# Optimization experiments

Measured on AMD Instinct MI355X. Metric: run time of the kernel, lower is better.

## Reference

```python
import jax, jax.numpy as jnp
import numpy as np

N = 100000
E = 1600000
CARDS = [1000, 100, 50, 10000]
EDIMS = [10, 6, 5, 18]  # emb_dim_from_card = clip(round(1.8*card**0.25), 4, 24)
NUM_IN = 32
HID = 128
EPS = 1e-5


def setup_inputs() -> dict:
    key = jax.random.key(0)
    ks = jax.random.split(key, 24)
    x_num = jax.random.normal(ks[0], (N, NUM_IN), dtype=jnp.float32)
    cols = [jax.random.randint(jax.random.fold_in(ks[1], j), (N,), 0, c) for j, c in enumerate(CARDS)]
    x_cat = jnp.stack(cols, axis=1)
    edge_index = jax.random.randint(ks[2], (2, E), 0, N)
    embs = {f"emb{j}": 0.02 * jax.random.normal(ks[3 + j], (c, d), dtype=jnp.float32)
            for j, (c, d) in enumerate(zip(CARDS, EDIMS))}
    in_dim = NUM_IN + sum(EDIMS)  # 71
    def lin(k, fi, fo):
        s = 1.0 / np.sqrt(fi)
        return jax.random.uniform(k, (fi, fo), jnp.float32, -s, s)
    params = dict(
        w_in=lin(ks[7], in_dim, HID), b_in=jnp.zeros((HID,), jnp.float32),
        w1l=lin(ks[8], HID, HID), b1l=jnp.zeros((HID,), jnp.float32), w1r=lin(ks[9], HID, HID),
        w2l=lin(ks[10], HID, HID), b2l=jnp.zeros((HID,), jnp.float32), w2r=lin(ks[11], HID, HID),
        g1=jnp.ones((HID,), jnp.float32), be1=jnp.zeros((HID,), jnp.float32),
        g2=jnp.ones((HID,), jnp.float32), be2=jnp.zeros((HID,), jnp.float32),
        wh1=lin(ks[12], HID, 64), bh1=jnp.zeros((64,), jnp.float32),
        wh2=lin(ks[13], 64, 1), bh2=jnp.zeros((1,), jnp.float32),
    )
    return {"x_num": x_num, "x_cat": x_cat, "edge_index": edge_index, **embs, **params}


def _layer_norm(x, g, b):
    mu = jnp.mean(x, axis=-1, keepdims=True)
    var = jnp.var(x, axis=-1, keepdims=True)
    return (x - mu) * jax.lax.rsqrt(var + EPS) * g + b


def _sage_conv(x, src, dst, wl, bl, wr):
    # PyG SAGEConv(mean): lin_l(mean_{j in N(i)} x_j) + lin_r(x_i)
    agg = jax.ops.segment_sum(x[src], dst, num_segments=N)
    cnt = jax.ops.segment_sum(jnp.ones((src.shape[0],), x.dtype), dst, num_segments=N)
    mean = agg / jnp.maximum(cnt, 1.0)[:, None]
    return mean @ wl + bl + x @ wr


def reference(x_num, x_cat, edge_index,
              emb0, emb1, emb2, emb3,
              w_in, b_in, w1l, b1l, w1r, w2l, b2l, w2r,
              g1, be1, g2, be2, wh1, bh1, wh2, bh2):
    # eval mode: dropout is identity
    zc = jnp.concatenate([emb0[x_cat[:, 0]], emb1[x_cat[:, 1]],
                          emb2[x_cat[:, 2]], emb3[x_cat[:, 3]]], axis=1)
    x = jnp.concatenate([x_num, zc], axis=1)
    x = jax.nn.relu(x @ w_in + b_in)
    src, dst = edge_index[0], edge_index[1]
    x1 = jax.nn.relu(_layer_norm(_sage_conv(x, src, dst, w1l, b1l, w1r), g1, be1))
    x = x + 0.5 * x1
    x2 = jax.nn.relu(_layer_norm(_sage_conv(x, src, dst, w2l, b2l, w2r), g2, be2))
    x = x + 0.5 * x2
    h = jax.nn.relu(x @ wh1 + bh1)
    return (h @ wh2 + bh2)[:, 0]
```

## Files before the change

kernel.cpp:

```cpp
#include <hip/hip_runtime.h>

#define HID 128

typedef __attribute__((ext_vector_type(8))) short short8;
typedef __attribute__((ext_vector_type(4))) float f32x4;

__device__ __forceinline__ float bf2f(unsigned short u) {
    unsigned int x = ((unsigned int)u) << 16;
    return __builtin_bit_cast(float, x);
}
__device__ __forceinline__ unsigned short f2bf(float f) {
    unsigned int u = __builtin_bit_cast(unsigned int, f);
    u += 0x7fffu + ((u >> 16) & 1u);
    return (unsigned short)(u >> 16);
}

__device__ __forceinline__ void prep_one(const float* __restrict__ s1, int k1,
    const float* __restrict__ s2, int N, int i,
    unsigned short* __restrict__ whi, unsigned short* __restrict__ wlo)
{
    int k = i / N, nn = i - k * N;
    float v = (k < k1) ? s1[(size_t)k * N + nn]
                       : (s2 ? s2[(size_t)(k - k1) * N + nn] : 0.f);
    unsigned short h = f2bf(v);
    unsigned short l = f2bf(v - bf2f(h));
    size_t o = ((size_t)(k >> 5) * N + nn) * 32 + (k & 31);
    whi[o] = h; wlo[o] = l;
}

__global__ __launch_bounds__(256) void k_prep(
    const float* __restrict__ w_in, const float* __restrict__ w1l,
    const float* __restrict__ w1r, const float* __restrict__ w2l,
    const float* __restrict__ w2r, const float* __restrict__ wh1,
    unsigned short* __restrict__ w0h, unsigned short* __restrict__ w0l,
    unsigned short* __restrict__ w1h, unsigned short* __restrict__ w1lo,
    unsigned short* __restrict__ w2h, unsigned short* __restrict__ w2lo,
    unsigned short* __restrict__ whh, unsigned short* __restrict__ whl,
    unsigned short* __restrict__ z1, unsigned short* __restrict__ z2,
    int* __restrict__ gCur)
{
    int b = blockIdx.x, t = threadIdx.x;
    if (b < 48) {
        prep_one(w_in, 71, nullptr, 128, b * 256 + t, w0h, w0l);
    } else if (b < 176) {
        prep_one(w1l, 128, w1r, 128, (b - 48) * 256 + t, w1h, w1lo);
    } else if (b < 304) {
        prep_one(w2l, 128, w2r, 128, (b - 176) * 256 + t, w2h, w2lo);
    } else if (b < 336) {
        prep_one(wh1, 128, nullptr, 64, (b - 304) * 256 + t, whh, whl);
    } else {
        z1[t] = 0; z2[t] = 0;
        gCur[t] = 0; gCur[t + 256] = 0;
    }
}

__global__ __launch_bounds__(256) void k_stack0(
    const float* __restrict__ xnum, const int* __restrict__ xcat,
    const float* __restrict__ e0, const float* __restrict__ e1,
    const float* __restrict__ e2, const float* __restrict__ e3,
    unsigned short* __restrict__ A0, int n)
{
    int g = blockIdx.x * 256 + threadIdx.x;
    int r = g / 6, c = g - r * 6;
    if (r >= n) return;
    int4 cc = ((const int4*)xcat)[r];
    float v[16];
    int base = c * 16;
    #pragma unroll
    for (int j = 0; j < 16; ++j) {
        int col = base + j;
        float val;
        if      (col < 32) val = xnum[(size_t)r * 32 + col];
        else if (col < 42) val = e0[(size_t)cc.x * 10 + (col - 32)];
        else if (col < 48) val = e1[(size_t)cc.y * 6  + (col - 42)];
        else if (col < 53) val = e2[(size_t)cc.z * 5  + (col - 48)];
        else if (col < 71) val = e3[(size_t)cc.w * 18 + (col - 53)];
        else               val = 0.f;
        v[j] = val;
    }
    unsigned int ph[8];
    #pragma unroll
    for (int j = 0; j < 8; ++j)
        ph[j] = (unsigned int)f2bf(v[2*j]) | ((unsigned int)f2bf(v[2*j+1]) << 16);
    unsigned int* dh = (unsigned int*)(A0 + (size_t)r * 96 + base);
    uint4 a; a.x = ph[0]; a.y = ph[1]; a.z = ph[2]; a.w = ph[3];
    uint4 b; b.x = ph[4]; b.y = ph[5]; b.z = ph[6]; b.w = ph[7];
    ((uint4*)dh)[0] = a; ((uint4*)dh)[1] = b;
}

__global__ __launch_bounds__(256) void k_part(const int* __restrict__ esrc,
    const int* __restrict__ edst, int* __restrict__ gCur, int2* __restrict__ ebuf,
    int ecount, int chunk, int cap)
{
    __shared__ int hist[512];
    __shared__ int base[512];
    int t = threadIdx.x;
    hist[t] = 0; hist[t + 256] = 0;
    __syncthreads();
    int start = blockIdx.x * chunk;
    int end = start + chunk < ecount ? start + chunk : ecount;
    for (int i = start + t; i < end; i += 256)
        atomicAdd(&hist[edst[i] >> 8], 1);
    __syncthreads();
    for (int bk = t; bk < 512; bk += 256) {
        int h = hist[bk];
        base[bk] = h ? atomicAdd(&gCur[bk], h) : 0;
        hist[bk] = 0;
    }
    __syncthreads();
    for (int i = start + t; i < end; i += 256) {
        int d = edst[i];
        int b = d >> 8;
        int slot = atomicAdd(&hist[b], 1);
        int pos = base[b] + slot;
        if (pos < cap)
            ebuf[(size_t)b * cap + pos] = make_int2(esrc[i], d);
    }
}

__global__ __launch_bounds__(512) void k_scanb(const int* __restrict__ gCur,
    int* __restrict__ bBase, int* __restrict__ row_ptr, int nbuck, int n, int ecount)
{
    __shared__ int sm[512];
    int t = threadIdx.x;
    int c = (t < nbuck) ? gCur[t] : 0;
    sm[t] = c;
    __syncthreads();
    for (int d = 1; d < 512; d <<= 1) {
        int v = (t >= d) ? sm[t - d] : 0;
        __syncthreads();
        sm[t] += v;
        __syncthreads();
    }
    if (t < nbuck) bBase[t] = sm[t] - c;
    if (t == 0) row_ptr[n] = ecount;
}

__global__ __launch_bounds__(256) void k_bcsr(const int2* __restrict__ ebuf,
    const int* __restrict__ gCur, const int* __restrict__ bBase,
    int* __restrict__ row_ptr, int* __restrict__ col, int cap, int n)
{
    __shared__ int h[256];
    __shared__ int sm[256];
    int b = blockIdx.x, t = threadIdx.x;
    int cnt = gCur[b];
    int nb0 = b << 8;
    const int2* eb = ebuf + (size_t)b * cap;
    h[t] = 0;
    __syncthreads();
    for (int i = t; i < cnt; i += 256)
        atomicAdd(&h[eb[i].y & 255], 1);
    __syncthreads();
    int hv = h[t];
    sm[t] = hv;
    __syncthreads();
    for (int d = 1; d < 256; d <<= 1) {
        int v = (t >= d) ? sm[t - d] : 0;
        __syncthreads();
        sm[t] += v;
        __syncthreads();
    }
    int excl = sm[t] - hv;
    int gb = bBase[b];
    int g = nb0 + t;
    if (g < n) row_ptr[g] = gb + excl;
    __syncthreads();
    h[t] = excl;
    __syncthreads();
    for (int i = t; i < cnt; i += 256) {
        int2 e = eb[i];
        int slot = atomicAdd(&h[e.y & 255], 1);
        col[gb + slot] = e.x;
    }
}

__global__ __launch_bounds__(256) void k_agg(
    const unsigned short* __restrict__ xh, unsigned short* __restrict__ mh, int SK,
    const int* __restrict__ row_ptr, const int* __restrict__ col, int n,
    int zr, int emax)
{
    int lane = threadIdx.x & 63;
    int qw  = lane >> 4;
    int l16 = lane & 15;
    int node = blockIdx.x * 4 + (threadIdx.x >> 6);
    if (node >= n) return;
    node = __builtin_amdgcn_readfirstlane(node);
    int s = row_ptr[node], e = row_ptr[node + 1];
    int deg = e - s;
    float a0 = 0.f, a1 = 0.f, a2 = 0.f, a3 = 0.f;
    float a4 = 0.f, a5 = 0.f, a6 = 0.f, a7 = 0.f;
    size_t cOff = (size_t)l16 * 8;

    auto accum = [&](uint4 r) {
        a0 += __builtin_bit_cast(float, r.x << 16);
        a1 += __builtin_bit_cast(float, r.x & 0xffff0000u);
        a2 += __builtin_bit_cast(float, r.y << 16);
        a3 += __builtin_bit_cast(float, r.y & 0xffff0000u);
        a4 += __builtin_bit_cast(float, r.z << 16);
        a5 += __builtin_bit_cast(float, r.z & 0xffff0000u);
        a6 += __builtin_bit_cast(float, r.w << 16);
        a7 += __builtin_bit_cast(float, r.w & 0xffff0000u);
    };

    int em1 = emax - 1;
    for (int p = s + qw; p < e; p += 16) {
        int p1 = p + 4, p2 = p + 8, p3 = p + 12;
        int q1 = p1 < em1 ? p1 : em1;
        int q2 = p2 < em1 ? p2 : em1;
        int q3 = p3 < em1 ? p3 : em1;
        int t0 = col[p];
        int t1 = col[q1];
        int t2 = col[q2];
        int t3 = col[q3];
        int c0 = t0;
        int c1 = (p1 < e) ? t1 : zr;
        int c2 = (p2 < e) ? t2 : zr;
        int c3 = (p3 < e) ? t3 : zr;
        uint4 r0 = *(const uint4*)(xh + (size_t)c0 * SK + cOff);
        uint4 r1 = *(const uint4*)(xh + (size_t)c1 * SK + cOff);
        uint4 r2 = *(const uint4*)(xh + (size_t)c2 * SK + cOff);
        uint4 r3 = *(const uint4*)(xh + (size_t)c3 * SK + cOff);
        accum(r0); accum(r1); accum(r2); accum(r3);
    }

    a0 += __shfl_xor(a0, 16); a0 += __shfl_xor(a0, 32);
    a1 += __shfl_xor(a1, 16); a1 += __shfl_xor(a1, 32);
    a2 += __shfl_xor(a2, 16); a2 += __shfl_xor(a2, 32);
    a3 += __shfl_xor(a3, 16); a3 += __shfl_xor(a3, 32);
    a4 += __shfl_xor(a4, 16); a4 += __shfl_xor(a4, 32);
    a5 += __shfl_xor(a5, 16); a5 += __shfl_xor(a5, 32);
    a6 += __shfl_xor(a6, 16); a6 += __shfl_xor(a6, 32);
    a7 += __shfl_xor(a7, 16); a7 += __shfl_xor(a7, 32);

    if (qw == 0) {
        float inv = 1.f / (float)(deg > 1 ? deg : 1);
        uint4 o;
        o.x = (unsigned int)f2bf(a0 * inv) | ((unsigned int)f2bf(a1 * inv) << 16);
        o.y = (unsigned int)f2bf(a2 * inv) | ((unsigned int)f2bf(a3 * inv) << 16);
        o.z = (unsigned int)f2bf(a4 * inv) | ((unsigned int)f2bf(a5 * inv) << 16);
        o.w = (unsigned int)f2bf(a6 * inv) | ((unsigned int)f2bf(a7 * inv) << 16);
        *(uint4*)(mh + (size_t)node * SK + cOff) = o;
    }
}

template<int NC, int KT8, int EPI>
__global__ __launch_bounds__(256) void k_gemm(
    const unsigned short* __restrict__ A, int SK,
    const unsigned short* __restrict__ Whi, const unsigned short* __restrict__ Wlo,
    const float* __restrict__ bias,
    const float* __restrict__ g, const float* __restrict__ be,
    const unsigned short* __restrict__ Src, int SSK,
    unsigned short* __restrict__ Dst, int DSK,
    const float* __restrict__ wh2, const float* __restrict__ bh2, float* __restrict__ outp,
    int n)
{
    constexpr int NT = NC / 64;
    __shared__ float Cb[32][NC + 4];
    int t = threadIdx.x;
    int lane = t & 63, w = t >> 6;
    int l15 = lane & 15, kg = lane >> 4;
    int m0 = blockIdx.x * 64;

    size_t aoff[4];
    #pragma unroll
    for (int mt = 0; mt < 4; ++mt) {
        int r = m0 + mt * 16 + l15;
        r = r < n ? r : n - 1;
        aoff[mt] = (size_t)r * SK + kg * 8;
    }
    size_t nb[NT];
    #pragma unroll
    for (int nt = 0; nt < NT; ++nt)
        nb[nt] = (size_t)(w * (NC / 4) + nt * 16 + l15) * 32 + kg * 8;

    f32x4 acc[4][NT];
    #pragma unroll
    for (int mt = 0; mt < 4; ++mt)
        #pragma unroll
        for (int nt = 0; nt < NT; ++nt)
            acc[mt][nt] = (f32x4)(0.f);

    #pragma unroll 1
    for (int s = 0; s < KT8; ++s) {
        int koff = s * 32;
        short8 ah[4];
        #pragma unroll
        for (int mt = 0; mt < 4; ++mt)
            ah[mt] = *(const short8*)(A + aoff[mt] + koff);
        short8 bh[NT], bl[NT];
        #pragma unroll
        for (int nt = 0; nt < NT; ++nt) {
            bh[nt] = *(const short8*)(Whi + (size_t)s * NC * 32 + nb[nt]);
            bl[nt] = *(const short8*)(Wlo + (size_t)s * NC * 32 + nb[nt]);
        }
        #pragma unroll
        for (int mt = 0; mt < 4; ++mt)
            #pragma unroll
            for (int nt = 0; nt < NT; ++nt)
                acc[mt][nt] = __builtin_amdgcn_mfma_f32_16x16x32_bf16(ah[mt], bh[nt], acc[mt][nt], 0, 0, 0);
        #pragma unroll
        for (int mt = 0; mt < 4; ++mt)
            #pragma unroll
            for (int nt = 0; nt < NT; ++nt)
                acc[mt][nt] = __builtin_amdgcn_mfma_f32_16x16x32_bf16(ah[mt], bl[nt], acc[mt][nt], 0, 0, 0);
    }

    constexpr int CW = NC / 8;
    int er = t >> 3, q = t & 7;
    int cb = q * CW;

    #pragma unroll
    for (int p = 0; p < 2; ++p) {
        if (p) __syncthreads();
        #pragma unroll
        for (int mt2 = 0; mt2 < 2; ++mt2) {
            int mt = 2 * p + mt2;
            #pragma unroll
            for (int nt = 0; nt < NT; ++nt)
                #pragma unroll
                for (int r = 0; r < 4; ++r)
                    Cb[mt2 * 16 + kg * 4 + r][w * (NC / 4) + nt * 16 + l15] = acc[mt][nt][r];
        }
        __syncthreads();

        int gr = m0 + p * 32 + er;

        if (EPI == 0) {
            if (gr < n) {
                #pragma unroll
                for (int i = 0; i < CW / 4; ++i) {
                    int c = cb + 4 * i;
                    float4 v  = *(const float4*)&Cb[er][c];
                    float4 bi = *(const float4*)&bias[c];
                    ushort4 hv = make_ushort4(f2bf(fmaxf(v.x + bi.x, 0.f)),
                                              f2bf(fmaxf(v.y + bi.y, 0.f)),
                                              f2bf(fmaxf(v.z + bi.z, 0.f)),
                                              f2bf(fmaxf(v.w + bi.w, 0.f)));
                    *(ushort4*)(Dst + (size_t)gr * DSK + c) = hv;
                }
            }
        } else if (EPI == 1) {
            float s = 0.f, ss = 0.f;
            #pragma unroll
            for (int i = 0; i < CW / 4; ++i) {
                int c = cb + 4 * i;
                float4 v  = *(const float4*)&Cb[er][c];
                float4 bi = *(const float4*)&bias[c];
                float a0 = v.x + bi.x, a1 = v.y + bi.y, a2 = v.z + bi.z, a3 = v.w + bi.w;
                s  += a0 + a1 + a2 + a3;
                ss += a0 * a0 + a1 * a1 + a2 * a2 + a3 * a3;
            }
            s  += __shfl_xor(s, 1);  s  += __shfl_xor(s, 2);  s  += __shfl_xor(s, 4);
            ss += __shfl_xor(ss, 1); ss += __shfl_xor(ss, 2); ss += __shfl_xor(ss, 4);
            float mu  = s * (1.f / NC);
            float var = ss * (1.f / NC) - mu * mu;
            float rs  = rsqrtf(var + 1e-5f);
            if (gr < n) {
                #pragma unroll
                for (int i = 0; i < CW / 4; ++i) {
                    int c = cb + 4 * i;
                    float4 v  = *(const float4*)&Cb[er][c];
                    float4 bi = *(const float4*)&bias[c];
                    float4 gg = *(const float4*)&g[c];
                    float4 bb = *(const float4*)&be[c];
                    float r0 = fmaxf((v.x + bi.x - mu) * rs * gg.x + bb.x, 0.f);
                    float r1 = fmaxf((v.y + bi.y - mu) * rs * gg.y + bb.y, 0.f);
                    float r2 = fmaxf((v.z + bi.z - mu) * rs * gg.z + bb.z, 0.f);
                    float r3 = fmaxf((v.w + bi.w - mu) * rs * gg.w + bb.w, 0.f);
                    ushort4 rh = *(const ushort4*)(Src + (size_t)gr * SSK + c);
                    ushort4 hv = make_ushort4(f2bf(bf2f(rh.x) + 0.5f * r0),
                                              f2bf(bf2f(rh.y) + 0.5f * r1),
                                              f2bf(bf2f(rh.z) + 0.5f * r2),
                                              f2bf(bf2f(rh.w) + 0.5f * r3));
                    *(ushort4*)(Dst + (size_t)gr * DSK + c) = hv;
                }
            }
        } else {
            float s = 0.f;
            #pragma unroll
            for (int i = 0; i < CW / 4; ++i) {
                int c = cb + 4 * i;
                float4 v  = *(const float4*)&Cb[er][c];
                float4 bi = *(const float4*)&bias[c];
                float4 w2 = *(const float4*)&wh2[c];
                s += fmaxf(v.x + bi.x, 0.f) * w2.x + fmaxf(v.y + bi.y, 0.f) * w2.y
                   + fmaxf(v.z + bi.z, 0.f) * w2.z + fmaxf(v.w + bi.w, 0.f) * w2.w;
            }
            s += __shfl_xor(s, 1); s += __shfl_xor(s, 2); s += __shfl_xor(s, 4);
            if (q == 0 && gr < n) outp[gr] = s + bh2[0];
        }
    }
}

extern "C" void kernel_launch(void* const* d_in, const int* in_sizes, int n_in,
                              void* d_out, int out_size, void* d_ws, size_t ws_size,
                              hipStream_t stream)
{
    const float* xnum = (const float*)d_in[0];
    const int*   xcat = (const int*)d_in[1];
    const int*   eidx = (const int*)d_in[2];
    const float* e0   = (const float*)d_in[3];
    const float* e1   = (const float*)d_in[4];
    const float* e2   = (const float*)d_in[5];
    const float* e3   = (const float*)d_in[6];
    const float* w_in = (const float*)d_in[7];
    const float* b_in = (const float*)d_in[8];
    const float* w1l  = (const float*)d_in[9];
    const float* b1l  = (const float*)d_in[10];
    const float* w1r  = (const float*)d_in[11];
    const float* w2l  = (const float*)d_in[12];
    const float* b2l  = (const float*)d_in[13];
    const float* w2r  = (const float*)d_in[14];
    const float* g1   = (const float*)d_in[15];
    const float* be1  = (const float*)d_in[16];
    const float* g2   = (const float*)d_in[17];
    const float* be2  = (const float*)d_in[18];
    const float* wh1  = (const float*)d_in[19];
    const float* bh1  = (const float*)d_in[20];
    const float* wh2  = (const float*)d_in[21];
    const float* bh2  = (const float*)d_in[22];

    int n = in_sizes[0] / 32;
    int ecount = in_sizes[2] / 2;
    const int* esrc = eidx;
    const int* edst = eidx + ecount;

    char* ws = (char*)d_ws;
    size_t off = 0;
    auto alloc = [&](size_t bytes) -> void* {
        void* p = ws + off;
        off += (bytes + 255) & ~(size_t)255;
        return p;
    };
    unsigned short* A1 = (unsigned short*)alloc((size_t)(n + 1) * 256 * 2);
    unsigned short* A3 = A1;
    unsigned short* A2 = (unsigned short*)alloc((size_t)(n + 1) * 256 * 2);
    unsigned short* A0 = A2;
    unsigned short* w0h = (unsigned short*)alloc((size_t)96 * 128 * 2);
    unsigned short* w0l = (unsigned short*)alloc((size_t)96 * 128 * 2);
    unsigned short* w1h = (unsigned short*)alloc((size_t)256 * 128 * 2);
    unsigned short* w1lo= (unsigned short*)alloc((size_t)256 * 128 * 2);
    unsigned short* w2h = (unsigned short*)alloc((size_t)256 * 128 * 2);
    unsigned short* w2lo= (unsigned short*)alloc((size_t)256 * 128 * 2);
    unsigned short* whh = (unsigned short*)alloc((size_t)128 * 64 * 2);
    unsigned short* whl = (unsigned short*)alloc((size_t)128 * 64 * 2);
    int nbuck = (n + 255) >> 8;
    int cap = ecount / nbuck + ecount / (2 * nbuck) + 256;
    int* gCur    = (int*)alloc(512 * 4);
    int* bBase   = (int*)alloc(512 * 4);
    int* row_ptr = (int*)alloc((size_t)(n + 1) * 4);
    int* col     = (int*)alloc((size_t)ecount * 4);
    int2* ebuf   = (int2*)alloc((size_t)nbuck * cap * 8);
    (void)ws_size; (void)n_in; (void)out_size;

    int gemmBlocks = (n + 63) / 64;
    int aggBlocks = (n + 3) / 4;

    k_prep<<<337, 256, 0, stream>>>(
        w_in, w1l, w1r, w2l, w2r, wh1,
        w0h, w0l, w1h, w1lo, w2h, w2lo, whh, whl,
        A1 + (size_t)n * 256, A2 + (size_t)n * 256, gCur);

    k_stack0<<<((size_t)n * 6 + 255) / 256, 256, 0, stream>>>(xnum, xcat, e0, e1, e2, e3, A0, n);

    int nblkP = 512;
    int chunk = (ecount + nblkP - 1) / nblkP;
    k_part<<<nblkP, 256, 0, stream>>>(esrc, edst, gCur, ebuf, ecount, chunk, cap);
    k_scanb<<<1, 512, 0, stream>>>(gCur, bBase, row_ptr, nbuck, n, ecount);
    k_bcsr<<<nbuck, 256, 0, stream>>>(ebuf, gCur, bBase, row_ptr, col, cap, n);

    k_gemm<128, 3, 0><<<gemmBlocks, 256, 0, stream>>>(
        A0, 96, w0h, w0l, b_in,
        nullptr, nullptr, nullptr, 0,
        A1 + 128, 256,
        nullptr, nullptr, nullptr, n);

    k_agg<<<aggBlocks, 256, 0, stream>>>(A1 + 128, A1, 256, row_ptr, col, n, n, ecount);
    k_gemm<128, 8, 1><<<gemmBlocks, 256, 0, stream>>>(
        A1, 256, w1h, w1lo, b1l,
        g1, be1, A1 + 128, 256,
        A2 + 128, 256,
        nullptr, nullptr, nullptr, n);

    k_agg<<<aggBlocks, 256, 0, stream>>>(A2 + 128, A2, 256, row_ptr, col, n, n, ecount);
    k_gemm<128, 8, 1><<<gemmBlocks, 256, 0, stream>>>(
        A2, 256, w2h, w2lo, b2l,
        g2, be2, A2 + 128, 256,
        A3, 128,
        nullptr, nullptr, nullptr, n);

    k_gemm<64, 4, 2><<<gemmBlocks, 256, 0, stream>>>(
        A3, 128, whh, whl, bh1,
        nullptr, nullptr, nullptr, 0,
        nullptr, 0,
        wh2, bh2, (float*)d_out, n);
}
```

Baseline: 434.3 us.

## Fuse head MLP into second SAGE layer GEMM epilogue

The final head GEMM kernel is folded into the epilogue of the layer-2 GEMM. The residual output tile stays in shared memory and is multiplied by the head weights with MFMA in-block, then reduced to the scalar output. This removes one kernel launch and the round trip of writing and re-reading the 100000x128 bf16 intermediate. The cost is extra shared memory, extra syncs per sub-tile, and more register pressure in the layer-2 kernel.

```diff
diff --git a/kernel.cpp b/kernel.cpp
--- a/kernel.cpp
+++ b/kernel.cpp
@@ -251,11 +251,15 @@
     const float* __restrict__ g, const float* __restrict__ be,
     const unsigned short* __restrict__ Src, int SSK,
     unsigned short* __restrict__ Dst, int DSK,
+    const unsigned short* __restrict__ Hh, const unsigned short* __restrict__ Hl,
+    const float* __restrict__ bh1p,
     const float* __restrict__ wh2, const float* __restrict__ bh2, float* __restrict__ outp,
     int n)
 {
     constexpr int NT = NC / 64;
     __shared__ float Cb[32][NC + 4];
+    __shared__ unsigned short Xs[(EPI == 3) ? 32 : 1][(EPI == 3) ? 132 : 1];
+    __shared__ float hq[(EPI == 3) ? 4 : 1][(EPI == 3) ? 32 : 1];
     int t = threadIdx.x;
     int lane = t & 63, w = t >> 6;
     int l15 = lane & 15, kg = lane >> 4;
@@ -339,7 +343,7 @@
                     *(ushort4*)(Dst + (size_t)gr * DSK + c) = hv;
                 }
             }
-        } else if (EPI == 1) {
+        } else {
             float s = 0.f, ss = 0.f;
             #pragma unroll
             for (int i = 0; i < CW / 4; ++i) {
@@ -355,7 +359,8 @@
             float mu  = s * (1.f / NC);
             float var = ss * (1.f / NC) - mu * mu;
             float rs  = rsqrtf(var + 1e-5f);
-            if (gr < n) {
+            int rl = gr < n ? gr : n - 1;
+            if (EPI == 3 || gr < n) {
                 #pragma unroll
                 for (int i = 0; i < CW / 4; ++i) {
                     int c = cb + 4 * i;
@@ -367,27 +372,59 @@
                     float r1 = fmaxf((v.y + bi.y - mu) * rs * gg.y + bb.y, 0.f);
                     float r2 = fmaxf((v.z + bi.z - mu) * rs * gg.z + bb.z, 0.f);
                     float r3 = fmaxf((v.w + bi.w - mu) * rs * gg.w + bb.w, 0.f);
-                    ushort4 rh = *(const ushort4*)(Src + (size_t)gr * SSK + c);
+                    ushort4 rh = *(const ushort4*)(Src + (size_t)rl * SSK + c);
                     ushort4 hv = make_ushort4(f2bf(bf2f(rh.x) + 0.5f * r0),
                                               f2bf(bf2f(rh.y) + 0.5f * r1),
                                               f2bf(bf2f(rh.z) + 0.5f * r2),
                                               f2bf(bf2f(rh.w) + 0.5f * r3));
-                    *(ushort4*)(Dst + (size_t)gr * DSK + c) = hv;
+                    if (EPI == 3)
+                        *(ushort4*)&Xs[er][c] = hv;
+                    else
+                        *(ushort4*)(Dst + (size_t)gr * DSK + c) = hv;
                 }
             }
-        } else {
-            float s = 0.f;
+        }
+
+        if (EPI == 3) {
+            __syncthreads();
+            f32x4 hacc[2];
+            hacc[0] = (f32x4)(0.f);
+            hacc[1] = (f32x4)(0.f);
             #pragma unroll
-            for (int i = 0; i < CW / 4; ++i) {
-                int c = cb + 4 * i;
-                float4 v  = *(const float4*)&Cb[er][c];
-                float4 bi = *(const float4*)&bias[c];
-                float4 w2 = *(const float4*)&wh2[c];
-                s += fmaxf(v.x + bi.x, 0.f) * w2.x + fmaxf(v.y + bi.y, 0.f) * w2.y
-                   + fmaxf(v.z + bi.z, 0.f) * w2.z + fmaxf(v.w + bi.w, 0.f) * w2.w;
+            for (int kt = 0; kt < NC / 32; ++kt) {
+                short8 af[2];
+                #pragma unroll
+                for (int mt = 0; mt < 2; ++mt)
+                    af[mt] = *(const short8*)&Xs[mt * 16 + l15][kt * 32 + kg * 8];
+                size_t ho = ((size_t)kt * 64 + w * 16 + l15) * 32 + kg * 8;
+                short8 bhh = *(const short8*)(Hh + ho);
+                short8 bhl = *(const short8*)(Hl + ho);
+                #pragma unroll
+                for (int mt = 0; mt < 2; ++mt)
+                    hacc[mt] = __builtin_amdgcn_mfma_f32_16x16x32_bf16(af[mt], bhh, hacc[mt], 0, 0, 0);
+                #pragma unroll
+                for (int mt = 0; mt < 2; ++mt)
+                    hacc[mt] = __builtin_amdgcn_mfma_f32_16x16x32_bf16(af[mt], bhl, hacc[mt], 0, 0, 0);
             }
-            s += __shfl_xor(s, 1); s += __shfl_xor(s, 2); s += __shfl_xor(s, 4);
-            if (q == 0 && gr < n) outp[gr] = s + bh2[0];
+            float b1v = bh1p[w * 16 + l15];
+            float w2v = wh2[w * 16 + l15];
+            #pragma unroll
+            for (int mt = 0; mt < 2; ++mt)
+                #pragma unroll
+                for (int r = 0; r < 4; ++r) {
+                    float part = fmaxf(hacc[mt][r] + b1v, 0.f) * w2v;
+                    part += __shfl_xor(part, 1);
+                    part += __shfl_xor(part, 2);
+                    part += __shfl_xor(part, 4);
+                    part += __shfl_xor(part, 8);
+                    if (l15 == 0) hq[w][mt * 16 + kg * 4 + r] = part;
+                }
+            __syncthreads();
+            if (t < 32) {
+                int gr2 = m0 + p * 32 + t;
+                if (gr2 < n)
+                    outp[gr2] = hq[0][t] + hq[1][t] + hq[2][t] + hq[3][t] + bh2[0];
+            }
         }
     }
 }
@@ -433,7 +470,6 @@
         return p;
     };
     unsigned short* A1 = (unsigned short*)alloc((size_t)(n + 1) * 256 * 2);
-    unsigned short* A3 = A1;
     unsigned short* A2 = (unsigned short*)alloc((size_t)(n + 1) * 256 * 2);
     unsigned short* A0 = A2;
     unsigned short* w0h = (unsigned short*)alloc((size_t)96 * 128 * 2);
@@ -473,25 +509,19 @@
         A0, 96, w0h, w0l, b_in,
         nullptr, nullptr, nullptr, 0,
         A1 + 128, 256,
-        nullptr, nullptr, nullptr, n);
+        nullptr, nullptr, nullptr, nullptr, nullptr, nullptr, n);
 
     k_agg<<<aggBlocks, 256, 0, stream>>>(A1 + 128, A1, 256, row_ptr, col, n, n, ecount);
     k_gemm<128, 8, 1><<<gemmBlocks, 256, 0, stream>>>(
         A1, 256, w1h, w1lo, b1l,
         g1, be1, A1 + 128, 256,
         A2 + 128, 256,
-        nullptr, nullptr, nullptr, n);
+        nullptr, nullptr, nullptr, nullptr, nullptr, nullptr, n);
 
     k_agg<<<aggBlocks, 256, 0, stream>>>(A2 + 128, A2, 256, row_ptr, col, n, n, ecount);
-    k_gemm<128, 8, 1><<<gemmBlocks, 256, 0, stream>>>(
+    k_gemm<128, 8, 3><<<gemmBlocks, 256, 0, stream>>>(
         A2, 256, w2h, w2lo, b2l,
         g2, be2, A2 + 128, 256,
-        A3, 128,
-        nullptr, nullptr, nullptr, n);
-
-    k_gemm<64, 4, 2><<<gemmBlocks, 256, 0, stream>>>(
-        A3, 128, whh, whl, bh1,
-        nullptr, nullptr, nullptr, 0,
         nullptr, 0,
-        wh2, bh2, (float*)d_out, n);
-}
+        whh, whl, bh1, wh2, bh2, (float*)d_out, n);
+}
```

New measurement: 442.7 us. No clear change (+1.9%).

## Merge independent preprocessing kernels into heterogeneous multi-role launches

Applied to the files above, without the earlier changes.

Combines edge partitioning with input stacking in one launch, and the first GEMM with CSR bucket construction in another. The single-block bucket scan is dropped; each CSR block now computes its own bucket base by reducing gCur, and row_ptr[n] is written in the prep kernel. The goal is fewer kernel launches and serialization gaps, letting independent work overlap on the GPU. The cost is redundant per-block prefix reductions and mixed-role blocks that may unbalance scheduling.

```diff
diff --git a/kernel.cpp b/kernel.cpp
--- a/kernel.cpp
+++ b/kernel.cpp
@@ -37,7 +37,7 @@
     unsigned short* __restrict__ w2h, unsigned short* __restrict__ w2lo,
     unsigned short* __restrict__ whh, unsigned short* __restrict__ whl,
     unsigned short* __restrict__ z1, unsigned short* __restrict__ z2,
-    int* __restrict__ gCur)
+    int* __restrict__ gCur, int* __restrict__ row_ptr, int n, int ecount)
 {
     int b = blockIdx.x, t = threadIdx.x;
     if (b < 48) {
@@ -51,126 +51,208 @@
     } else {
         z1[t] = 0; z2[t] = 0;
         gCur[t] = 0; gCur[t + 256] = 0;
-    }
-}
-
-__global__ __launch_bounds__(256) void k_stack0(
+        if (t == 0) row_ptr[n] = ecount;
+    }
+}
+
+__global__ __launch_bounds__(256) void k_m1(
+    const int* __restrict__ esrc, const int* __restrict__ edst,
+    int* __restrict__ gCur, int2* __restrict__ ebuf, int ecount, int chunk, int cap,
     const float* __restrict__ xnum, const int* __restrict__ xcat,
     const float* __restrict__ e0, const float* __restrict__ e1,
     const float* __restrict__ e2, const float* __restrict__ e3,
     unsigned short* __restrict__ A0, int n)
 {
-    int g = blockIdx.x * 256 + threadIdx.x;
-    int r = g / 6, c = g - r * 6;
-    if (r >= n) return;
-    int4 cc = ((const int4*)xcat)[r];
-    float v[16];
-    int base = c * 16;
-    #pragma unroll
-    for (int j = 0; j < 16; ++j) {
-        int col = base + j;
-        float val;
-        if      (col < 32) val = xnum[(size_t)r * 32 + col];
-        else if (col < 42) val = e0[(size_t)cc.x * 10 + (col - 32)];
-        else if (col < 48) val = e1[(size_t)cc.y * 6  + (col - 42)];
-        else if (col < 53) val = e2[(size_t)cc.z * 5  + (col - 48)];
-        else if (col < 71) val = e3[(size_t)cc.w * 18 + (col - 53)];
-        else               val = 0.f;
-        v[j] = val;
-    }
-    unsigned int ph[8];
-    #pragma unroll
-    for (int j = 0; j < 8; ++j)
-        ph[j] = (unsigned int)f2bf(v[2*j]) | ((unsigned int)f2bf(v[2*j+1]) << 16);
-    unsigned int* dh = (unsigned int*)(A0 + (size_t)r * 96 + base);
-    uint4 a; a.x = ph[0]; a.y = ph[1]; a.z = ph[2]; a.w = ph[3];
-    uint4 b; b.x = ph[4]; b.y = ph[5]; b.z = ph[6]; b.w = ph[7];
-    ((uint4*)dh)[0] = a; ((uint4*)dh)[1] = b;
-}
-
-__global__ __launch_bounds__(256) void k_part(const int* __restrict__ esrc,
-    const int* __restrict__ edst, int* __restrict__ gCur, int2* __restrict__ ebuf,
-    int ecount, int chunk, int cap)
-{
     __shared__ int hist[512];
     __shared__ int base[512];
     int t = threadIdx.x;
-    hist[t] = 0; hist[t + 256] = 0;
-    __syncthreads();
-    int start = blockIdx.x * chunk;
-    int end = start + chunk < ecount ? start + chunk : ecount;
-    for (int i = start + t; i < end; i += 256)
-        atomicAdd(&hist[edst[i] >> 8], 1);
-    __syncthreads();
-    for (int bk = t; bk < 512; bk += 256) {
-        int h = hist[bk];
-        base[bk] = h ? atomicAdd(&gCur[bk], h) : 0;
-        hist[bk] = 0;
-    }
-    __syncthreads();
-    for (int i = start + t; i < end; i += 256) {
-        int d = edst[i];
-        int b = d >> 8;
-        int slot = atomicAdd(&hist[b], 1);
-        int pos = base[b] + slot;
-        if (pos < cap)
-            ebuf[(size_t)b * cap + pos] = make_int2(esrc[i], d);
-    }
-}
-
-__global__ __launch_bounds__(512) void k_scanb(const int* __restrict__ gCur,
-    int* __restrict__ bBase, int* __restrict__ row_ptr, int nbuck, int n, int ecount)
-{
-    __shared__ int sm[512];
+    if (blockIdx.x < 512) {
+        hist[t] = 0; hist[t + 256] = 0;
+        __syncthreads();
+        int start = blockIdx.x * chunk;
+        int end = start + chunk < ecount ? start + chunk : ecount;
+        for (int i = start + t; i < end; i += 256)
+            atomicAdd(&hist[edst[i] >> 8], 1);
+        __syncthreads();
+        for (int bk = t; bk < 512; bk += 256) {
+            int h = hist[bk];
+            base[bk] = h ? atomicAdd(&gCur[bk], h) : 0;
+            hist[bk] = 0;
+        }
+        __syncthreads();
+        for (int i = start + t; i < end; i += 256) {
+            int d = edst[i];
+            int b = d >> 8;
+            int slot = atomicAdd(&hist[b], 1);
+            int pos = base[b] + slot;
+            if (pos < cap)
+                ebuf[(size_t)b * cap + pos] = make_int2(esrc[i], d);
+        }
+    } else {
+        int g = (blockIdx.x - 512) * 256 + t;
+        int r = g / 6, c = g - r * 6;
+        if (r >= n) return;
+        int4 cc = ((const int4*)xcat)[r];
+        float v[16];
+        int cbase = c * 16;
+        #pragma unroll
+        for (int j = 0; j < 16; ++j) {
+            int col = cbase + j;
+            float val;
+            if      (col < 32) val = xnum[(size_t)r * 32 + col];
+            else if (col < 42) val = e0[(size_t)cc.x * 10 + (col - 32)];
+            else if (col < 48) val = e1[(size_t)cc.y * 6  + (col - 42)];
+            else if (col < 53) val = e2[(size_t)cc.z * 5  + (col - 48)];
+            else if (col < 71) val = e3[(size_t)cc.w * 18 + (col - 53)];
+            else               val = 0.f;
+            v[j] = val;
+        }
+        unsigned int ph[8];
+        #pragma unroll
+        for (int j = 0; j < 8; ++j)
+            ph[j] = (unsigned int)f2bf(v[2*j]) | ((unsigned int)f2bf(v[2*j+1]) << 16);
+        unsigned int* dh = (unsigned int*)(A0 + (size_t)r * 96 + cbase);
+        uint4 a; a.x = ph[0]; a.y = ph[1]; a.z = ph[2]; a.w = ph[3];
+        uint4 bb; bb.x = ph[4]; bb.y = ph[5]; bb.z = ph[6]; bb.w = ph[7];
+        ((uint4*)dh)[0] = a; ((uint4*)dh)[1] = bb;
+    }
+}
+
+__global__ __launch_bounds__(256) void k_m2(
+    const unsigned short* __restrict__ A,
+    const unsigned short* __restrict__ Whi, const unsigned short* __restrict__ Wlo,
+    const float* __restrict__ bias,
+    unsigned short* __restrict__ Dst,
+    int n, int gemmBlocks,
+    const int2* __restrict__ ebuf, const int* __restrict__ gCur,
+    int* __restrict__ row_ptr, int* __restrict__ col, int cap)
+{
+    __shared__ float Cb[32][132];
+    __shared__ int h2[256];
+    __shared__ int sm2[256];
     int t = threadIdx.x;
-    int c = (t < nbuck) ? gCur[t] : 0;
-    sm[t] = c;
-    __syncthreads();
-    for (int d = 1; d < 512; d <<= 1) {
-        int v = (t >= d) ? sm[t - d] : 0;
-        __syncthreads();
-        sm[t] += v;
-        __syncthreads();
-    }
-    if (t < nbuck) bBase[t] = sm[t] - c;
-    if (t == 0) row_ptr[n] = ecount;
-}
-
-__global__ __launch_bounds__(256) void k_bcsr(const int2* __restrict__ ebuf,
-    const int* __restrict__ gCur, const int* __restrict__ bBase,
-    int* __restrict__ row_ptr, int* __restrict__ col, int cap, int n)
-{
-    __shared__ int h[256];
-    __shared__ int sm[256];
-    int b = blockIdx.x, t = threadIdx.x;
-    int cnt = gCur[b];
-    int nb0 = b << 8;
-    const int2* eb = ebuf + (size_t)b * cap;
-    h[t] = 0;
-    __syncthreads();
-    for (int i = t; i < cnt; i += 256)
-        atomicAdd(&h[eb[i].y & 255], 1);
-    __syncthreads();
-    int hv = h[t];
-    sm[t] = hv;
-    __syncthreads();
-    for (int d = 1; d < 256; d <<= 1) {
-        int v = (t >= d) ? sm[t - d] : 0;
-        __syncthreads();
-        sm[t] += v;
-        __syncthreads();
-    }
-    int excl = sm[t] - hv;
-    int gb = bBase[b];
-    int g = nb0 + t;
-    if (g < n) row_ptr[g] = gb + excl;
-    __syncthreads();
-    h[t] = excl;
-    __syncthreads();
-    for (int i = t; i < cnt; i += 256) {
-        int2 e = eb[i];
-        int slot = atomicAdd(&h[e.y & 255], 1);
-        col[gb + slot] = e.x;
+
+    if ((int)blockIdx.x < gemmBlocks) {
+        int lane = t & 63, w = t >> 6;
+        int l15 = lane & 15, kg = lane >> 4;
+        int m0 = blockIdx.x * 64;
+
+        size_t aoff[4];
+        #pragma unroll
+        for (int mt = 0; mt < 4; ++mt) {
+            int r = m0 + mt * 16 + l15;
+            r = r < n ? r : n - 1;
+            aoff[mt] = (size_t)r * 96 + kg * 8;
+        }
+        size_t nb[2];
+        #pragma unroll
+        for (int nt = 0; nt < 2; ++nt)
+            nb[nt] = (size_t)(w * 32 + nt * 16 + l15) * 32 + kg * 8;
+
+        f32x4 acc[4][2];
+        #pragma unroll
+        for (int mt = 0; mt < 4; ++mt)
+            #pragma unroll
+            for (int nt = 0; nt < 2; ++nt)
+                acc[mt][nt] = (f32x4)(0.f);
+
+        #pragma unroll 1
+        for (int s = 0; s < 3; ++s) {
+            int koff = s * 32;
+            short8 ah[4];
+            #pragma unroll
+            for (int mt = 0; mt < 4; ++mt)
+                ah[mt] = *(const short8*)(A + aoff[mt] + koff);
+            short8 bh[2], bl[2];
+            #pragma unroll
+            for (int nt = 0; nt < 2; ++nt) {
+                bh[nt] = *(const short8*)(Whi + (size_t)s * 128 * 32 + nb[nt]);
+                bl[nt] = *(const short8*)(Wlo + (size_t)s * 128 * 32 + nb[nt]);
+            }
+            #pragma unroll
+            for (int mt = 0; mt < 4; ++mt)
+                #pragma unroll
+                for (int nt = 0; nt < 2; ++nt)
+                    acc[mt][nt] = __builtin_amdgcn_mfma_f32_16x16x32_bf16(ah[mt], bh[nt], acc[mt][nt], 0, 0, 0);
+            #pragma unroll
+            for (int mt = 0; mt < 4; ++mt)
+                #pragma unroll
+                for (int nt = 0; nt < 2; ++nt)
+                    acc[mt][nt] = __builtin_amdgcn_mfma_f32_16x16x32_bf16(ah[mt], bl[nt], acc[mt][nt], 0, 0, 0);
+        }
+
+        int er = t >> 3, q = t & 7;
+        int cb = q * 16;
+        #pragma unroll
+        for (int p = 0; p < 2; ++p) {
+            if (p) __syncthreads();
+            #pragma unroll
+            for (int mt2 = 0; mt2 < 2; ++mt2) {
+                int mt = 2 * p + mt2;
+                #pragma unroll
+                for (int nt = 0; nt < 2; ++nt)
+                    #pragma unroll
+                    for (int r = 0; r < 4; ++r)
+                        Cb[mt2 * 16 + kg * 4 + r][w * 32 + nt * 16 + l15] = acc[mt][nt][r];
+            }
+            __syncthreads();
+            int gr = m0 + p * 32 + er;
+            if (gr < n) {
+                #pragma unroll
+                for (int i = 0; i < 4; ++i) {
+                    int c = cb + 4 * i;
+                    float4 v  = *(const float4*)&Cb[er][c];
+                    float4 bi = *(const float4*)&bias[c];
+                    ushort4 hv = make_ushort4(f2bf(fmaxf(v.x + bi.x, 0.f)),
+                                              f2bf(fmaxf(v.y + bi.y, 0.f)),
+                                              f2bf(fmaxf(v.z + bi.z, 0.f)),
+                                              f2bf(fmaxf(v.w + bi.w, 0.f)));
+                    *(ushort4*)(Dst + (size_t)gr * 256 + c) = hv;
+                }
+            }
+        }
+    } else {
+        int b = blockIdx.x - gemmBlocks;
+        int partial = 0;
+        if (t < b) partial += gCur[t];
+        if (t + 256 < b) partial += gCur[t + 256];
+        sm2[t] = partial;
+        __syncthreads();
+        for (int d = 128; d > 0; d >>= 1) {
+            if (t < d) sm2[t] += sm2[t + d];
+            __syncthreads();
+        }
+        int gb = sm2[0];
+        __syncthreads();
+
+        int cnt = gCur[b];
+        int nb0 = b << 8;
+        const int2* eb = ebuf + (size_t)b * cap;
+        h2[t] = 0;
+        __syncthreads();
+        for (int i = t; i < cnt; i += 256)
+            atomicAdd(&h2[eb[i].y & 255], 1);
+        __syncthreads();
+        int hv = h2[t];
+        sm2[t] = hv;
+        __syncthreads();
+        for (int d = 1; d < 256; d <<= 1) {
+            int v = (t >= d) ? sm2[t - d] : 0;
+            __syncthreads();
+            sm2[t] += v;
+            __syncthreads();
+        }
+        int excl = sm2[t] - hv;
+        int g = nb0 + t;
+        if (g < n) row_ptr[g] = gb + excl;
+        __syncthreads();
+        h2[t] = excl;
+        __syncthreads();
+        for (int i = t; i < cnt; i += 256) {
+            int2 e = eb[i];
+            int slot = atomicAdd(&h2[e.y & 255], 1);
+            col[gb + slot] = e.x;
+        }
     }
 }
 
@@ -325,21 +407,7 @@
 
         int gr = m0 + p * 32 + er;
 
-        if (EPI == 0) {
-            if (gr < n) {
-                #pragma unroll
-                for (int i = 0; i < CW / 4; ++i) {
-                    int c = cb + 4 * i;
-                    float4 v  = *(const float4*)&Cb[er][c];
-                    float4 bi = *(const float4*)&bias[c];
-                    ushort4 hv = make_ushort4(f2bf(fmaxf(v.x + bi.x, 0.f)),
-                                              f2bf(fmaxf(v.y + bi.y, 0.f)),
-                                              f2bf(fmaxf(v.z + bi.z, 0.f)),
-                                              f2bf(fmaxf(v.w + bi.w, 0.f)));
-                    *(ushort4*)(Dst + (size_t)gr * DSK + c) = hv;
-                }
-            }
-        } else if (EPI == 1) {
+        if (EPI == 1) {
             float s = 0.f, ss = 0.f;
             #pragma unroll
             for (int i = 0; i < CW / 4; ++i) {
@@ -447,7 +515,6 @@
     int nbuck = (n + 255) >> 8;
     int cap = ecount / nbuck + ecount / (2 * nbuck) + 256;
     int* gCur    = (int*)alloc(512 * 4);
-    int* bBase   = (int*)alloc(512 * 4);
     int* row_ptr = (int*)alloc((size_t)(n + 1) * 4);
     int* col     = (int*)alloc((size_t)ecount * 4);
     int2* ebuf   = (int2*)alloc((size_t)nbuck * cap * 8);
@@ -455,25 +522,22 @@
 
     int gemmBlocks = (n + 63) / 64;
     int aggBlocks = (n + 3) / 4;
+    int stackBlocks = ((size_t)n * 6 + 255) / 256;
+    int nblkP = 512;
+    int chunk = (ecount + nblkP - 1) / nblkP;
 
     k_prep<<<337, 256, 0, stream>>>(
         w_in, w1l, w1r, w2l, w2r, wh1,
         w0h, w0l, w1h, w1lo, w2h, w2lo, whh, whl,
-        A1 + (size_t)n * 256, A2 + (size_t)n * 256, gCur);
-
-    k_stack0<<<((size_t)n * 6 + 255) / 256, 256, 0, stream>>>(xnum, xcat, e0, e1, e2, e3, A0, n);
-
-    int nblkP = 512;
-    int chunk = (ecount + nblkP - 1) / nblkP;
-    k_part<<<nblkP, 256, 0, stream>>>(esrc, edst, gCur, ebuf, ecount, chunk, cap);
-    k_scanb<<<1, 512, 0, stream>>>(gCur, bBase, row_ptr, nbuck, n, ecount);
-    k_bcsr<<<nbuck, 256, 0, stream>>>(ebuf, gCur, bBase, row_ptr, col, cap, n);
-
-    k_gemm<128, 3, 0><<<gemmBlocks, 256, 0, stream>>>(
-        A0, 96, w0h, w0l, b_in,
-        nullptr, nullptr, nullptr, 0,
-        A1 + 128, 256,
-        nullptr, nullptr, nullptr, n);
+        A1 + (size_t)n * 256, A2 + (size_t)n * 256, gCur, row_ptr, n, ecount);
+
+    k_m1<<<512 + stackBlocks, 256, 0, stream>>>(
+        esrc, edst, gCur, ebuf, ecount, chunk, cap,
+        xnum, xcat, e0, e1, e2, e3, A0, n);
+
+    k_m2<<<gemmBlocks + nbuck, 256, 0, stream>>>(
+        A0, w0h, w0l, b_in, A1 + 128, n, gemmBlocks,
+        ebuf, gCur, row_ptr, col, cap);
 
     k_agg<<<aggBlocks, 256, 0, stream>>>(A1 + 128, A1, 256, row_ptr, col, n, n, ecount);
     k_gemm<128, 8, 1><<<gemmBlocks, 256, 0, stream>>>(
```

After: 423.1 us. -2.6%, faster.
